# Kernel optimization log

Hardware: AMD Instinct MI355X
Metric: run time of the kernel (lower is better)

## Reference

```python
import jax, jax.numpy as jnp
import numpy as np

BETA = 0.5      # Tukey power transform exponent (args['beta'])
EPS = 1e-12     # F.normalize eps


def setup_inputs() -> dict:
    key = jax.random.key(0)
    k1, k2, k3 = jax.random.split(key, 3)
    B, C, D = 512, 200, 768
    raw_features = jax.random.normal(k1, (B, D), jnp.float32)
    class_means = jax.random.normal(k2, (C, D), jnp.float32)
    # Build SPD-like stacked inverse covariances [C, D, D] (as pinv of a
    # shrunk+normalized covariance would be symmetric PSD).
    A = jax.random.normal(k3, (C, D, D), jnp.float32) / jnp.sqrt(D)
    inv_covs = jnp.einsum('cij,ckj->cik', A, A) + 0.1 * jnp.eye(D, dtype=jnp.float32)
    return {
        'raw_features': raw_features,
        'class_means': class_means,
        'inv_covs': inv_covs,
        'active_classes': C,
    }


def reference(raw_features, class_means, inv_covs, active_classes):
    # Tukey transform: sign(x) * |x|^beta  (applied once, not per class)
    v = jnp.sign(raw_features) * jnp.abs(raw_features) ** BETA          # [B, D]
    # L2 normalize features (once) and class means
    v = v / jnp.clip(jnp.linalg.norm(v, axis=-1, keepdims=True), EPS)
    m = class_means / jnp.clip(
        jnp.linalg.norm(class_means, axis=-1, keepdims=True), EPS)      # [C, D]
    diff = v[:, None, :] - m[None, :, :]                                # [B, C, D]
    # Batched Mahalanobis quadratic form: all classes in one fused contraction
    left = jnp.einsum('bcd,cde->bce', diff, inv_covs)                   # [B, C, D]
    mahal = jnp.sum(left * diff, axis=-1)                               # [B, C]
    return -mahal
```

## Files before the change

kernel.cpp:

```cpp
#include <hip/hip_runtime.h>


#define B_SZ 512
#define C_SZ 200
#define D_SZ 768
#define NK   24

typedef __bf16 bf16x8 __attribute__((ext_vector_type(8)));
typedef float  f32x4  __attribute__((ext_vector_type(4)));

__device__ __forceinline__ void gl16(const __bf16* g, __bf16* l) {
    __builtin_amdgcn_global_load_lds(
        (const __attribute__((address_space(1))) void*)g,
        (__attribute__((address_space(3))) void*)l, 16, 0, 0);
}

__global__ __launch_bounds__(256)
void fecam_prep(const float* __restrict__ raw, const float* __restrict__ cmeans,
                float* __restrict__ v_out, float* __restrict__ m_out,
                __bf16* __restrict__ vt, float* __restrict__ out)
{
    const int blk = blockIdx.x;
    const int tid = threadIdx.x;
    if (blk >= B_SZ + C_SZ) {
        const int base = (blk - (B_SZ + C_SZ)) * 1024;
        #pragma unroll
        for (int i = 0; i < 4; ++i) {
            int idx = base + i * 256 + tid;
            if (idx < B_SZ * C_SZ) out[idx] = 0.0f;
        }
        return;
    }
    const bool isf = (blk < B_SZ);
    const float* src = isf ? raw + (size_t)blk * D_SZ
                           : cmeans + (size_t)(blk - B_SZ) * D_SZ;
    float vals[3]; float ss = 0.f;
    #pragma unroll
    for (int i = 0; i < 3; ++i) {
        float xx = src[tid + i * 256];
        if (isf) xx = copysignf(sqrtf(fabsf(xx)), xx);
        vals[i] = xx; ss += xx * xx;
    }
    #pragma unroll
    for (int off = 32; off; off >>= 1) ss += __shfl_xor(ss, off);
    __shared__ float red[4];
    if ((tid & 63) == 0) red[tid >> 6] = ss;
    __syncthreads();
    const float inv = 1.0f / fmaxf(sqrtf(red[0] + red[1] + red[2] + red[3]), 1e-12f);
    if (isf) {
        const int b = blk;
        #pragma unroll
        for (int i = 0; i < 3; ++i) {
            const int e = tid + i * 256;
            const float val = vals[i] * inv;
            v_out[(size_t)b * D_SZ + e] = val;
            const int idx = ((b >> 7) * NK + (e >> 5)) * 4096
                          + ((e >> 3) & 3) * 1024 + (b & 127) * 8 + (e & 7);
            vt[idx] = (__bf16)val;
        }
    } else {
        float* dst = m_out + (size_t)(blk - B_SZ) * D_SZ;
        #pragma unroll
        for (int i = 0; i < 3; ++i) dst[tid + i * 256] = vals[i] * inv;
    }
}

__global__ __launch_bounds__(256, 2)
void fecam_mahal(const float* __restrict__ v, const float* __restrict__ m,
                 const __bf16* __restrict__ vt, const float* __restrict__ invc,
                 float* __restrict__ out)
{
    __shared__ __bf16 As[2][4096];
    __shared__ __bf16 Bs[2][4096];
    __shared__ float  ms[D_SZ];
    __shared__ float  reds[4];

    const int rr = blockIdx.x;
    const int x  = rr & 7, tt = rr >> 3;
    const int rb = tt & 3, pg = tt >> 2;
    const int p  = pg * 8 + x;
    const int c  = p / 6, dt = p - c * 6;
    const int b0 = rb * 128, d0 = dt * 128;

    const int tid = threadIdx.x;
    const int lane = tid & 63, w = tid >> 6;
    const int wr = w >> 1, wc = w & 1;
    const int l15 = lane & 15, g = lane >> 4;
    const int drow = tid >> 1, eh = tid & 1;

    const float*  bsrc  = invc + (size_t)c * D_SZ * D_SZ + (size_t)(d0 + drow) * D_SZ + eh * 16;
    const __bf16* atile = vt + (size_t)rb * NK * 4096 + tid * 8;
    const float*  mrow  = m + (size_t)c * D_SZ;

    ms[tid]       = mrow[tid];
    ms[tid + 256] = mrow[tid + 256];
    ms[tid + 512] = mrow[tid + 512];

    float4 vb[4];
    float  sacc = 0.f;
    f32x4  acc[4][4] = {};

    auto issueB = [&](int kk) {
        const float* s = bsrc + kk * 32;
        vb[0] = *(const float4*)(s);
        vb[1] = *(const float4*)(s + 4);
        vb[2] = *(const float4*)(s + 8);
        vb[3] = *(const float4*)(s + 12);
    };
    auto gloadA = [&](int kk, int buf) {
        const __bf16* s = atile + kk * 4096;
        gl16(s,        &As[buf][tid * 8]);
        gl16(s + 2048, &As[buf][tid * 8 + 2048]);
    };
    auto writeB = [&](int buf, int kk) {
        float f[16];
        #pragma unroll
        for (int i = 0; i < 4; ++i) {
            f[i*4+0] = vb[i].x; f[i*4+1] = vb[i].y;
            f[i*4+2] = vb[i].z; f[i*4+3] = vb[i].w;
        }
        const float* mse = &ms[kk * 32 + eh * 16];
        float sl = 0.f;
        #pragma unroll
        for (int i = 0; i < 16; ++i) sl += f[i] * mse[i];
        sacc += sl;
        bf16x8 p0, p1;
        #pragma unroll
        for (int i = 0; i < 8; ++i) { p0[i] = (__bf16)f[i]; p1[i] = (__bf16)f[8+i]; }
        *(bf16x8*)&Bs[buf][(eh*2 + 0) * 1024 + drow * 8] = p0;
        *(bf16x8*)&Bs[buf][(eh*2 + 1) * 1024 + drow * 8] = p1;
    };
    auto mfmaPhase = [&](int buf) {
        bf16x8 afr[4], bfr[4];
        #pragma unroll
        for (int mm = 0; mm < 4; ++mm)
            afr[mm] = *(const bf16x8*)&As[buf][g * 1024 + (wr*64 + mm*16 + l15) * 8];
        #pragma unroll
        for (int nn = 0; nn < 4; ++nn)
            bfr[nn] = *(const bf16x8*)&Bs[buf][g * 1024 + (wc*64 + nn*16 + l15) * 8];
        #pragma unroll
        for (int mm = 0; mm < 4; ++mm)
            #pragma unroll
            for (int nn = 0; nn < 4; ++nn)
                acc[mm][nn] = __builtin_amdgcn_mfma_f32_16x16x32_bf16(
                    afr[mm], bfr[nn], acc[mm][nn], 0, 0, 0);
    };

    issueB(0);
    gloadA(0, 0);
    __syncthreads();
    writeB(0, 0);
    __syncthreads();
    issueB(1);

    int cur = 0;
    for (int k = 0; k < NK; ++k) {
        if (k + 1 < NK) gloadA(k + 1, cur ^ 1);
        mfmaPhase(cur);
        if (k + 1 < NK) writeB(cur ^ 1, k + 1);
        if (k + 1 < NK) __syncthreads();
        if (k + 2 < NK) issueB(k + 2);
        cur ^= 1;
    }

    float sthr = ms[d0 + drow] * sacc;
    #pragma unroll
    for (int off = 1; off < 64; off <<= 1) sthr += __shfl_xor(sthr, off);
    if (lane == 0) reds[w] = sthr;
    __syncthreads();
    const float s_part = reds[0] + reds[1] + reds[2] + reds[3];

    const int dbase = d0 + wc * 64 + l15;
    float md2[4];
    #pragma unroll
    for (int nn = 0; nn < 4; ++nn) md2[nn] = 2.0f * ms[dbase - d0 + d0 + nn * 16];
    #pragma unroll
    for (int mm = 0; mm < 4; ++mm) {
        #pragma unroll
        for (int j = 0; j < 4; ++j) {
            const int b = b0 + wr * 64 + mm * 16 + g * 4 + j;
            const float* vrow = v + (size_t)b * D_SZ + dbase;
            float val = 0.f;
            #pragma unroll
            for (int nn = 0; nn < 4; ++nn)
                val += acc[mm][nn][j] * (md2[nn] - vrow[nn * 16]);
            val += __shfl_xor(val, 1);
            val += __shfl_xor(val, 2);
            val += __shfl_xor(val, 4);
            val += __shfl_xor(val, 8);
            if (l15 == 0)
                atomicAdd(&out[(size_t)b * C_SZ + c], (wc == 0) ? (val - s_part) : val);
        }
    }
}

extern "C" void kernel_launch(void* const* d_in, const int* in_sizes, int n_in,
                              void* d_out, int out_size, void* d_ws, size_t ws_size,
                              hipStream_t stream)
{
    const float* raw    = (const float*)d_in[0];
    const float* cmeans = (const float*)d_in[1];
    const float* invc   = (const float*)d_in[2];
    float* out = (float*)d_out;

    float*  v  = (float*)d_ws;
    float*  mn = v + (size_t)B_SZ * D_SZ;
    __bf16* vt = (__bf16*)(mn + (size_t)C_SZ * D_SZ);

    fecam_prep<<<B_SZ + C_SZ + 100, 256, 0, stream>>>(raw, cmeans, v, mn, vt, out);
    fecam_mahal<<<4800, 256, 0, stream>>>(v, mn, vt, invc, out);
}
```

Baseline: 876.3 us.

## Cover all batch rows per block and stream fp32 inverse covariance directly to LDS

New measurement: 805.0 us. 1.09x faster.

```diff
diff --git a/kernel.cpp b/kernel.cpp
--- a/kernel.cpp
+++ b/kernel.cpp
@@ -5,11 +5,12 @@
 #define C_SZ 200
 #define D_SZ 768
 #define NK   24
+#define DD   (D_SZ * D_SZ)
 
 typedef __bf16 bf16x8 __attribute__((ext_vector_type(8)));
 typedef float  f32x4  __attribute__((ext_vector_type(4)));
 
-__device__ __forceinline__ void gl16(const __bf16* g, __bf16* l) {
+__device__ __forceinline__ void gl16(const void* g, void* l) {
     __builtin_amdgcn_global_load_lds(
         (const __attribute__((address_space(1))) void*)g,
         (__attribute__((address_space(3))) void*)l, 16, 0, 0);
@@ -54,8 +55,7 @@
             const int e = tid + i * 256;
             const float val = vals[i] * inv;
             v_out[(size_t)b * D_SZ + e] = val;
-            const int idx = ((b >> 7) * NK + (e >> 5)) * 4096
-                          + ((e >> 3) & 3) * 1024 + (b & 127) * 8 + (e & 7);
+            const int idx = (e >> 5) * 16384 + ((e >> 3) & 3) * 4096 + b * 8 + (e & 7);
             vt[idx] = (__bf16)val;
         }
     } else {
@@ -65,125 +65,133 @@
     }
 }
 
-__global__ __launch_bounds__(256, 2)
+__global__ __launch_bounds__(512, 2)
 void fecam_mahal(const float* __restrict__ v, const float* __restrict__ m,
                  const __bf16* __restrict__ vt, const float* __restrict__ invc,
                  float* __restrict__ out)
 {
-    __shared__ __bf16 As[2][4096];
-    __shared__ __bf16 Bs[2][4096];
+    __shared__ __bf16 As[2][16384];
+    __shared__ float  Bs[3][4096];
     __shared__ float  ms[D_SZ];
-    __shared__ float  reds[4];
-
-    const int rr = blockIdx.x;
-    const int x  = rr & 7, tt = rr >> 3;
-    const int rb = tt & 3, pg = tt >> 2;
-    const int p  = pg * 8 + x;
-    const int c  = p / 6, dt = p - c * 6;
-    const int b0 = rb * 128, d0 = dt * 128;
-
-    const int tid = threadIdx.x;
-    const int lane = tid & 63, w = tid >> 6;
-    const int wr = w >> 1, wc = w & 1;
-    const int l15 = lane & 15, g = lane >> 4;
-    const int drow = tid >> 1, eh = tid & 1;
-
-    const float*  bsrc  = invc + (size_t)c * D_SZ * D_SZ + (size_t)(d0 + drow) * D_SZ + eh * 16;
-    const __bf16* atile = vt + (size_t)rb * NK * 4096 + tid * 8;
-    const float*  mrow  = m + (size_t)c * D_SZ;
-
-    ms[tid]       = mrow[tid];
-    ms[tid + 256] = mrow[tid + 256];
-    ms[tid + 512] = mrow[tid + 512];
-
-    float4 vb[4];
-    float  sacc = 0.f;
-    f32x4  acc[4][4] = {};
-
-    auto issueB = [&](int kk) {
+    __shared__ float  reds[2];
+
+    const int bid = blockIdx.x;
+    const int c   = bid / 6;
+    const int dt  = bid - c * 6;
+    const int d0  = dt * 128;
+
+    const int tid  = threadIdx.x;
+    const int lane = tid & 63;
+    const int w    = tid >> 6;
+    const int wr   = w >> 1;
+    const int wc   = w & 1;
+    const int l15  = lane & 15;
+    const int g    = lane >> 4;
+
+    ms[tid] = m[(size_t)c * D_SZ + tid];
+    if (tid < 256) ms[512 + tid] = m[(size_t)c * D_SZ + 512 + tid];
+    __syncthreads();
+
+    const int brow = w * 16 + (lane >> 3);
+    const int bel  = (((lane & 7) ^ ((lane >> 3) & 7)) << 4) >> 2;
+    const float* bsrc = invc + (size_t)c * DD + (size_t)(d0 + brow) * D_SZ + bel;
+    const __bf16* asrc = vt + w * 2048 + lane * 8;
+
+    auto issueA = [&](int kk, int buf) {
+        const __bf16* s = asrc + kk * 16384;
+        char* d = (char*)&As[buf][0] + w * 4096;
+        #pragma unroll
+        for (int i = 0; i < 4; ++i) gl16(s + i * 512, d + i * 1024);
+    };
+    auto issueB = [&](int kk, int buf) {
         const float* s = bsrc + kk * 32;
-        vb[0] = *(const float4*)(s);
-        vb[1] = *(const float4*)(s + 4);
-        vb[2] = *(const float4*)(s + 8);
-        vb[3] = *(const float4*)(s + 12);
+        char* d = (char*)&Bs[buf][0] + w * 2048;
+        gl16(s, d);
+        gl16(s + 8 * D_SZ, d + 1024);
     };
-    auto gloadA = [&](int kk, int buf) {
-        const __bf16* s = atile + kk * 4096;
-        gl16(s,        &As[buf][tid * 8]);
-        gl16(s + 2048, &As[buf][tid * 8 + 2048]);
-    };
-    auto writeB = [&](int buf, int kk) {
-        float f[16];
-        #pragma unroll
-        for (int i = 0; i < 4; ++i) {
-            f[i*4+0] = vb[i].x; f[i*4+1] = vb[i].y;
-            f[i*4+2] = vb[i].z; f[i*4+3] = vb[i].w;
-        }
-        const float* mse = &ms[kk * 32 + eh * 16];
-        float sl = 0.f;
-        #pragma unroll
-        for (int i = 0; i < 16; ++i) sl += f[i] * mse[i];
-        sacc += sl;
-        bf16x8 p0, p1;
-        #pragma unroll
-        for (int i = 0; i < 8; ++i) { p0[i] = (__bf16)f[i]; p1[i] = (__bf16)f[8+i]; }
-        *(bf16x8*)&Bs[buf][(eh*2 + 0) * 1024 + drow * 8] = p0;
-        *(bf16x8*)&Bs[buf][(eh*2 + 1) * 1024 + drow * 8] = p1;
-    };
-    auto mfmaPhase = [&](int buf) {
-        bf16x8 afr[4], bfr[4];
-        #pragma unroll
-        for (int mm = 0; mm < 4; ++mm)
-            afr[mm] = *(const bf16x8*)&As[buf][g * 1024 + (wr*64 + mm*16 + l15) * 8];
-        #pragma unroll
-        for (int nn = 0; nn < 4; ++nn)
-            bfr[nn] = *(const bf16x8*)&Bs[buf][g * 1024 + (wc*64 + nn*16 + l15) * 8];
-        #pragma unroll
-        for (int mm = 0; mm < 4; ++mm)
+
+    f32x4 acc[8][4] = {};
+    float sacc0 = 0.f, sacc1 = 0.f, sacc2 = 0.f, sacc3 = 0.f;
+
+    issueB(0, 0); issueA(0, 0); issueB(1, 1);
+
+    for (int k = 0; k < NK; ++k) {
+        __builtin_amdgcn_s_barrier();
+        const int ka = (k + 1 < NK) ? k + 1 : NK - 1;
+        issueA(ka, (k + 1) & 1);
+        const int kb = (k + 2 < NK) ? k + 2 : NK - 1;
+        issueB(kb, (k + 2) % 3);
+        asm volatile("s_waitcnt vmcnt(8)" ::: "memory");
+        __builtin_amdgcn_s_barrier();
+        __builtin_amdgcn_sched_barrier(0);
+
+        const float* bb = &Bs[k % 3][0];
+        float bme[8];
+        if (w < 2) {
+            #pragma unroll
+            for (int i = 0; i < 8; ++i) bme[i] = ms[k * 32 + g * 8 + i];
+        }
+        bf16x8 bfr[4];
+        #pragma unroll
+        for (int nn = 0; nn < 4; ++nn) {
+            const int col = wc * 64 + nn * 16 + l15;
+            const int sw  = (col & 7) << 4;
+            const int o0  = (col * 128 + ((g * 32) ^ sw)) >> 2;
+            const int o1  = (col * 128 + ((g * 32 + 16) ^ sw)) >> 2;
+            const f32x4 b0 = *(const f32x4*)(bb + o0);
+            const f32x4 b1 = *(const f32x4*)(bb + o1);
+            bf16x8 t;
+            t[0] = (__bf16)b0[0]; t[1] = (__bf16)b0[1];
+            t[2] = (__bf16)b0[2]; t[3] = (__bf16)b0[3];
+            t[4] = (__bf16)b1[0]; t[5] = (__bf16)b1[1];
+            t[6] = (__bf16)b1[2]; t[7] = (__bf16)b1[3];
+            bfr[nn] = t;
+            if (w < 2) {
+                const float s = b0[0]*bme[0] + b0[1]*bme[1] + b0[2]*bme[2] + b0[3]*bme[3]
+                              + b1[0]*bme[4] + b1[1]*bme[5] + b1[2]*bme[6] + b1[3]*bme[7];
+                if      (nn == 0) sacc0 += s;
+                else if (nn == 1) sacc1 += s;
+                else if (nn == 2) sacc2 += s;
+                else              sacc3 += s;
+            }
+        }
+        const __bf16* ab = &As[k & 1][0];
+        #pragma unroll
+        for (int mm = 0; mm < 8; ++mm) {
+            const int row = wr * 128 + mm * 16 + l15;
+            const bf16x8 af = *(const bf16x8*)(ab + g * 4096 + row * 8);
             #pragma unroll
             for (int nn = 0; nn < 4; ++nn)
                 acc[mm][nn] = __builtin_amdgcn_mfma_f32_16x16x32_bf16(
-                    afr[mm], bfr[nn], acc[mm][nn], 0, 0, 0);
-    };
-
-    issueB(0);
-    gloadA(0, 0);
+                    af, bfr[nn], acc[mm][nn], 0, 0, 0);
+        }
+    }
+
+    if (w < 2) {
+        const int cb = d0 + wc * 64 + l15;
+        float s = ms[cb] * sacc0 + ms[cb + 16] * sacc1
+                + ms[cb + 32] * sacc2 + ms[cb + 48] * sacc3;
+        #pragma unroll
+        for (int off = 1; off < 64; off <<= 1) s += __shfl_xor(s, off);
+        if (lane == 0) reds[w] = s;
+    }
     __syncthreads();
-    writeB(0, 0);
-    __syncthreads();
-    issueB(1);
-
-    int cur = 0;
-    for (int k = 0; k < NK; ++k) {
-        if (k + 1 < NK) gloadA(k + 1, cur ^ 1);
-        mfmaPhase(cur);
-        if (k + 1 < NK) writeB(cur ^ 1, k + 1);
-        if (k + 1 < NK) __syncthreads();
-        if (k + 2 < NK) issueB(k + 2);
-        cur ^= 1;
-    }
-
-    float sthr = ms[d0 + drow] * sacc;
-    #pragma unroll
-    for (int off = 1; off < 64; off <<= 1) sthr += __shfl_xor(sthr, off);
-    if (lane == 0) reds[w] = sthr;
-    __syncthreads();
-    const float s_part = reds[0] + reds[1] + reds[2] + reds[3];
+    const float s_part = reds[0] + reds[1];
 
     const int dbase = d0 + wc * 64 + l15;
     float md2[4];
     #pragma unroll
-    for (int nn = 0; nn < 4; ++nn) md2[nn] = 2.0f * ms[dbase - d0 + d0 + nn * 16];
-    #pragma unroll
-    for (int mm = 0; mm < 4; ++mm) {
+    for (int nn = 0; nn < 4; ++nn) md2[nn] = 2.0f * ms[dbase + nn * 16];
+    #pragma unroll
+    for (int mm = 0; mm < 8; ++mm) {
         #pragma unroll
         for (int j = 0; j < 4; ++j) {
-            const int b = b0 + wr * 64 + mm * 16 + g * 4 + j;
+            const int b = wr * 128 + mm * 16 + g * 4 + j;
             const float* vrow = v + (size_t)b * D_SZ + dbase;
-            float val = 0.f;
-            #pragma unroll
-            for (int nn = 0; nn < 4; ++nn)
-                val += acc[mm][nn][j] * (md2[nn] - vrow[nn * 16]);
+            float val = acc[mm][0][j] * (md2[0] - vrow[0])
+                      + acc[mm][1][j] * (md2[1] - vrow[16])
+                      + acc[mm][2][j] * (md2[2] - vrow[32])
+                      + acc[mm][3][j] * (md2[3] - vrow[48]);
             val += __shfl_xor(val, 1);
             val += __shfl_xor(val, 2);
             val += __shfl_xor(val, 4);
@@ -203,10 +211,10 @@
     const float* invc   = (const float*)d_in[2];
     float* out = (float*)d_out;
 
-    float*  v  = (float*)d_ws;
-    float*  mn = v + (size_t)B_SZ * D_SZ;
+    float*  vf = (float*)d_ws;
+    float*  mn = vf + (size_t)B_SZ * D_SZ;
     __bf16* vt = (__bf16*)(mn + (size_t)C_SZ * D_SZ);
 
-    fecam_prep<<<B_SZ + C_SZ + 100, 256, 0, stream>>>(raw, cmeans, v, mn, vt, out);
-    fecam_mahal<<<4800, 256, 0, stream>>>(v, mn, vt, invc, out);
-}
+    fecam_prep<<<B_SZ + C_SZ + 100, 256, 0, stream>>>(raw, cmeans, vf, mn, vt, out);
+    fecam_mahal<<<C_SZ * 6, 512, 0, stream>>>(vf, mn, vt, invc, out);
+}
```
